# Optimization experiments

Measured on AMD Instinct MI355X. Metric: run time of the kernel, lower is better.

The kernel has to match this reference:

```python
import jax, jax.numpy as jnp
import numpy as np

EPS = jnp.finfo(jnp.float32).eps


def setup_inputs() -> dict:
    key = jax.random.key(0)
    k0, k1, k2 = jax.random.split(key, 3)
    B, N = 1, 4194304
    cloud_t0 = jax.random.normal(k0, (B, N, 3), dtype=jnp.float32)
    cloud_t1 = jax.random.normal(k1, (B, N, 3), dtype=jnp.float32)
    weights = jax.random.uniform(k2, (B, N), dtype=jnp.float32)
    return {"cloud_t0": cloud_t0, "cloud_t1": cloud_t1, "weights": weights}


def reference(cloud_t0, cloud_t1, weights):
    # use_epsilon_on_weights = False branch
    count_nonzero = jnp.sum(weights > 0.0, axis=-1)
    not_enough_points = count_nonzero < 3
    weights = weights + (not_enough_points.astype(weights.dtype) * EPS)[:, None]

    cum_wts = jnp.sum(weights, axis=-1)                      # (B,)
    w = weights[:, :, None]                                   # (B,N,1)
    mx = jnp.sum(cloud_t0 * w, axis=1) / cum_wts[:, None]     # (B,3) weighted centroid
    my = jnp.sum(cloud_t1 * w, axis=1) / cum_wts[:, None]
    Xc = cloud_t0 - mx[:, None, :]
    Yc = cloud_t1 - my[:, None, :]
    # weighted cross-covariance: (B,3,3)
    Sxy = jnp.einsum('bno,bni->boi', Yc * w, Xc) / cum_wts[:, None, None]

    U, D, Vh = jnp.linalg.svd(Sxy, full_matrices=False)       # torch.svd returns V = Vh^T
    V = jnp.swapaxes(Vh, -1, -2)

    # rank via torch.linalg.matrix_rank default tol: max_sv * max(m,n) * eps
    tol = D.max(axis=-1) * 3 * EPS
    rank = jnp.sum(D > tol[:, None], axis=-1)

    det_S = jnp.linalg.det(Sxy)
    det_mul = jnp.linalg.det(U) * jnp.linalg.det(V)
    sign_full = jnp.where(det_S < 0.0, -1.0, 1.0)             # rank == 3 case
    sign_def = jnp.where(jnp.isclose(det_mul, -1.0), -1.0, 1.0)  # rank == 2 case
    s = jnp.where(rank > 2, sign_full, sign_def)              # (B,)

    # R = U @ diag(1,1,s) @ V^T
    diag = jnp.stack([jnp.ones_like(s), jnp.ones_like(s), s], axis=-1)  # (B,3)
    R = jnp.einsum('boc,bc,bic->boi', U, diag, V)             # (B,3,3)
    t = my - jnp.einsum('boc,bc->bo', R, mx)                  # (B,3)

    B = R.shape[0]
    R4 = jnp.concatenate([R, jnp.zeros((B, 1, 3), R.dtype)], axis=1)    # (B,4,3)
    t4 = jnp.concatenate([t, jnp.ones((B, 1), t.dtype)], axis=-1)       # (B,4)
    T = jnp.concatenate([R4, t4[:, :, None]], axis=-1)        # (B,4,4)
    return T, not_enough_points
```

## Files before the change

### kernel.cpp

```cpp
#include <hip/hip_runtime.h>
#include <math.h>

#define NACC 32

typedef float f4 __attribute__((ext_vector_type(4)));


__device__ __forceinline__ void accum_point(float w, float x0, float x1, float x2,
                                            float y0, float y1, float y2, float* a) {
    a[0] += (w > 0.0f) ? 1.0f : 0.0f;
    a[1] += w;
    a[2] = fmaf(w, x0, a[2]); a[3] = fmaf(w, x1, a[3]); a[4] = fmaf(w, x2, a[4]);
    float wy0 = w * y0, wy1 = w * y1, wy2 = w * y2;
    a[5] += wy0; a[6] += wy1; a[7] += wy2;
    a[8]  = fmaf(wy0, x0, a[8]);  a[9]  = fmaf(wy0, x1, a[9]);  a[10] = fmaf(wy0, x2, a[10]);
    a[11] = fmaf(wy1, x0, a[11]); a[12] = fmaf(wy1, x1, a[12]); a[13] = fmaf(wy1, x2, a[13]);
    a[14] = fmaf(wy2, x0, a[14]); a[15] = fmaf(wy2, x1, a[15]); a[16] = fmaf(wy2, x2, a[16]);
    a[17] += x0; a[18] += x1; a[19] += x2;
    a[20] += y0; a[21] += y1; a[22] += y2;
    a[23] = fmaf(y0, x0, a[23]); a[24] = fmaf(y0, x1, a[24]); a[25] = fmaf(y0, x2, a[25]);
    a[26] = fmaf(y1, x0, a[26]); a[27] = fmaf(y1, x1, a[27]); a[28] = fmaf(y1, x2, a[28]);
    a[29] = fmaf(y2, x0, a[29]); a[30] = fmaf(y2, x1, a[30]); a[31] = fmaf(y2, x2, a[31]);
}

__device__ __forceinline__ double det3(const double m[3][3]) {
    return m[0][0] * (m[1][1] * m[2][2] - m[1][2] * m[2][1])
         - m[0][1] * (m[1][0] * m[2][2] - m[1][2] * m[2][0])
         + m[0][2] * (m[1][0] * m[2][1] - m[1][1] * m[2][0]);
}

__global__ __launch_bounds__(256) void kabsch_fused(
    const float* __restrict__ c0, const float* __restrict__ c1,
    const float* __restrict__ w, int N, float* __restrict__ acc32, int nblocks,
    unsigned* __restrict__ ticket, float* __restrict__ out) {
    __shared__ float wred[4][NACC];

    float a[NACC];
    #pragma unroll
    for (int i = 0; i < NACC; ++i) a[i] = 0.0f;

    const int t = threadIdx.x;
    const int lane = t & 63, wave = t >> 6;
    const f4* __restrict__ A4 = (const f4*)c0;
    const f4* __restrict__ B4 = (const f4*)c1;
    const f4* __restrict__ W4 = (const f4*)w;

    const int ngrp = N >> 2;
    const int stride = gridDim.x << 8;
    for (int g = (blockIdx.x << 8) + t; g < ngrp; g += stride) {
        int i3 = 3 * g;
        f4 a0 = A4[i3], a1 = A4[i3 + 1], a2 = A4[i3 + 2];
        f4 b0 = B4[i3], b1 = B4[i3 + 1], b2 = B4[i3 + 2];
        f4 vw = W4[g];
        accum_point(vw.x, a0.x, a0.y, a0.z, b0.x, b0.y, b0.z, a);
        accum_point(vw.y, a0.w, a1.x, a1.y, b0.w, b1.x, b1.y, a);
        accum_point(vw.z, a1.z, a1.w, a2.x, b1.z, b1.w, b2.x, a);
        accum_point(vw.w, a2.y, a2.z, a2.w, b2.y, b2.z, b2.w, a);
    }
    if (blockIdx.x == 0 && t == 0) {
        for (int i = (N >> 2) << 2; i < N; ++i)
            accum_point(w[i], c0[3*i], c0[3*i+1], c0[3*i+2],
                        c1[3*i], c1[3*i+1], c1[3*i+2], a);
    }

    {
        int hi;
        hi = lane & 1;
        #pragma unroll
        for (int i = 0; i < 16; ++i) {
            float send = hi ? a[i] : a[i + 16];
            float recv = __shfl_xor(send, 1, 64);
            a[i] = (hi ? a[i + 16] : a[i]) + recv;
        }
        hi = lane & 2;
        #pragma unroll
        for (int i = 0; i < 8; ++i) {
            float send = hi ? a[i] : a[i + 8];
            float recv = __shfl_xor(send, 2, 64);
            a[i] = (hi ? a[i + 8] : a[i]) + recv;
        }
        hi = lane & 4;
        #pragma unroll
        for (int i = 0; i < 4; ++i) {
            float send = hi ? a[i] : a[i + 4];
            float recv = __shfl_xor(send, 4, 64);
            a[i] = (hi ? a[i + 4] : a[i]) + recv;
        }
        hi = lane & 8;
        #pragma unroll
        for (int i = 0; i < 2; ++i) {
            float send = hi ? a[i] : a[i + 2];
            float recv = __shfl_xor(send, 8, 64);
            a[i] = (hi ? a[i + 2] : a[i]) + recv;
        }
        hi = lane & 16;
        {
            float send = hi ? a[0] : a[1];
            float recv = __shfl_xor(send, 16, 64);
            a[0] = (hi ? a[1] : a[0]) + recv;
        }
        a[0] += __shfl_xor(a[0], 32, 64);
    }
    if (lane < 32) {
        int acc = ((lane & 1) << 4) | ((lane & 2) << 2) | (lane & 4)
                | ((lane & 8) >> 2) | ((lane & 16) >> 4);
        wred[wave][acc] = a[0];
    }
    __syncthreads();

    if (t < NACC) {
        float val = wred[0][t] + wred[1][t] + wred[2][t] + wred[3][t];
        float* p = acc32 + t;
        asm volatile("global_atomic_add_f32 %0, %1, off"
                     :: "v"(p), "v"(val) : "memory");
    }
    asm volatile("s_waitcnt vmcnt(0)" ::: "memory");
    __syncthreads();
    __shared__ unsigned amlast;
    if (t == 0) amlast = atomicAdd(ticket, 1u);
    __syncthreads();
    if (amlast != (unsigned)(nblocks - 1)) return;

    __shared__ float tot[NACC];
    if (t < NACC) {
        float* p = acc32 + t;
        float zero = 0.0f, old;
        asm volatile("global_atomic_add_f32 %0, %1, %2, off sc0"
                     : "=&v"(old) : "v"(p), "v"(zero) : "memory");
        asm volatile("s_waitcnt vmcnt(0)" ::: "memory");
        tot[t] = old;
    }
    __syncthreads();
    if (t != 0) return;

    double d[NACC];
    #pragma unroll
    for (int i = 0; i < NACC; ++i) d[i] = (double)tot[i];

    const double EPSF = (double)1.1920929e-7f;
    double cnt = d[0];
    double W = d[1];
    double swx[3] = { d[2], d[3], d[4] };
    double swy[3] = { d[5], d[6], d[7] };
    double swyx[9];
    for (int i = 0; i < 9; ++i) swyx[i] = d[8 + i];
    bool nep = cnt < 3.0;
    if (nep) {
        W += EPSF * (double)N;
        for (int i = 0; i < 3; ++i) { swx[i] += EPSF * d[17 + i]; swy[i] += EPSF * d[20 + i]; }
        for (int i = 0; i < 9; ++i) swyx[i] += EPSF * d[23 + i];
    }

    double mx[3], my[3];
    for (int i = 0; i < 3; ++i) { mx[i] = swx[i] / W; my[i] = swy[i] / W; }
    double S[3][3];
    for (int o = 0; o < 3; ++o)
        for (int i = 0; i < 3; ++i)
            S[o][i] = swyx[o * 3 + i] / W - my[o] * mx[i];

    double Bm[3][3], V[3][3];
    for (int i = 0; i < 3; ++i)
        for (int j = 0; j < 3; ++j) {
            double acc = 0.0;
            for (int k = 0; k < 3; ++k) acc += S[k][i] * S[k][j];
            Bm[i][j] = acc;
            V[i][j] = (i == j) ? 1.0 : 0.0;
        }
    for (int sweep = 0; sweep < 30; ++sweep) {
        double off2 = Bm[0][1]*Bm[0][1] + Bm[0][2]*Bm[0][2] + Bm[1][2]*Bm[1][2];
        double diag2 = Bm[0][0]*Bm[0][0] + Bm[1][1]*Bm[1][1] + Bm[2][2]*Bm[2][2];
        if (off2 <= diag2 * 1e-32 + 1e-300) break;
        for (int pair = 0; pair < 3; ++pair) {
            int p = (pair == 2) ? 1 : 0;
            int q = (pair == 0) ? 1 : 2;
            double apq = Bm[p][q];
            if (fabs(apq) < 1e-300) continue;
            double theta = (Bm[q][q] - Bm[p][p]) / (2.0 * apq);
            double tt = ((theta >= 0.0) ? 1.0 : -1.0) / (fabs(theta) + sqrt(1.0 + theta * theta));
            double c = 1.0 / sqrt(1.0 + tt * tt);
            double sn = tt * c;
            for (int k = 0; k < 3; ++k) {
                double bkp = Bm[k][p], bkq = Bm[k][q];
                Bm[k][p] = c * bkp - sn * bkq;
                Bm[k][q] = sn * bkp + c * bkq;
            }
            for (int k = 0; k < 3; ++k) {
                double bpk = Bm[p][k], bqk = Bm[q][k];
                Bm[p][k] = c * bpk - sn * bqk;
                Bm[q][k] = sn * bpk + c * bqk;
            }
            for (int k = 0; k < 3; ++k) {
                double vkp = V[k][p], vkq = V[k][q];
                V[k][p] = c * vkp - sn * vkq;
                V[k][q] = sn * vkp + c * vkq;
            }
        }
    }
    double lam[3] = { Bm[0][0], Bm[1][1], Bm[2][2] };
    for (int i = 0; i < 2; ++i)
        for (int j = i + 1; j < 3; ++j)
            if (lam[j] > lam[i]) {
                double tl = lam[i]; lam[i] = lam[j]; lam[j] = tl;
                for (int k = 0; k < 3; ++k) { double tv = V[k][i]; V[k][i] = V[k][j]; V[k][j] = tv; }
            }
    double sig[3];
    for (int i = 0; i < 3; ++i) sig[i] = sqrt(fmax(lam[i], 0.0));

    double U[3][3];
    for (int i = 0; i < 3; ++i) {
        double u0 = S[0][0]*V[0][i] + S[0][1]*V[1][i] + S[0][2]*V[2][i];
        double u1 = S[1][0]*V[0][i] + S[1][1]*V[1][i] + S[1][2]*V[2][i];
        double u2 = S[2][0]*V[0][i] + S[2][1]*V[1][i] + S[2][2]*V[2][i];
        double nrm = sqrt(u0*u0 + u1*u1 + u2*u2);
        if (nrm > 1e-150) {
            U[0][i] = u0 / nrm; U[1][i] = u1 / nrm; U[2][i] = u2 / nrm;
        } else if (i == 0) {
            U[0][0] = 1.0; U[1][0] = 0.0; U[2][0] = 0.0;
        } else if (i == 1) {
            double e0 = (fabs(U[0][0]) < 0.9) ? 1.0 : 0.0;
            double e1 = 1.0 - e0;
            double dp = e0 * U[0][0] + e1 * U[1][0];
            double v0 = e0 - dp * U[0][0], v1 = e1 - dp * U[1][0], v2 = -dp * U[2][0];
            double n2 = sqrt(v0*v0 + v1*v1 + v2*v2);
            U[0][1] = v0 / n2; U[1][1] = v1 / n2; U[2][1] = v2 / n2;
        } else {
            U[0][2] = U[1][0]*U[2][1] - U[2][0]*U[1][1];
            U[1][2] = U[2][0]*U[0][1] - U[0][0]*U[2][1];
            U[2][2] = U[0][0]*U[1][1] - U[1][0]*U[0][1];
        }
    }

    double tol = sig[0] * 3.0 * EPSF;
    int rank = (sig[0] > tol) + (sig[1] > tol) + (sig[2] > tol);
    double detS = det3(S);
    double det_mul = det3(U) * det3(V);
    double sign_full = (detS < 0.0) ? -1.0 : 1.0;
    double sign_def = (fabs(det_mul + 1.0) <= 1.00001e-5) ? -1.0 : 1.0;
    double s = (rank > 2) ? sign_full : sign_def;

    double R[3][3];
    for (int o = 0; o < 3; ++o)
        for (int i = 0; i < 3; ++i)
            R[o][i] = U[o][0]*V[i][0] + U[o][1]*V[i][1] + s * U[o][2]*V[i][2];
    double tv[3];
    for (int o = 0; o < 3; ++o)
        tv[o] = my[o] - (R[o][0]*mx[0] + R[o][1]*mx[1] + R[o][2]*mx[2]);

    for (int o = 0; o < 3; ++o) {
        out[o * 4 + 0] = (float)R[o][0];
        out[o * 4 + 1] = (float)R[o][1];
        out[o * 4 + 2] = (float)R[o][2];
        out[o * 4 + 3] = (float)tv[o];
    }
    out[12] = 0.0f; out[13] = 0.0f; out[14] = 0.0f; out[15] = 1.0f;
    out[16] = nep ? 1.0f : 0.0f;
}

extern "C" void kernel_launch(void* const* d_in, const int* in_sizes, int n_in,
                              void* d_out, int out_size, void* d_ws, size_t ws_size,
                              hipStream_t stream) {
    const float* c0 = (const float*)d_in[0];
    const float* c1 = (const float*)d_in[1];
    const float* w  = (const float*)d_in[2];
    float* out = (float*)d_out;
    int N = in_sizes[2];

    int ngrp = N >> 2;
    int blocks = (ngrp + 255) >> 8;
    if (blocks > 1024) blocks = 1024;
    if (blocks < 1) blocks = 1;

    float* acc32 = (float*)d_ws;
    unsigned* ticket = (unsigned*)((char*)d_ws + NACC * sizeof(float));

    hipMemsetAsync(d_ws, 0, NACC * sizeof(float) + sizeof(unsigned), stream);
    kabsch_fused<<<blocks, 256, 0, stream>>>(c0, c1, w, N, acc32, blocks, ticket, out);
}
```

Baseline: 150.7 us.

## Software-prefetch next grid-stride tile and pad global atomic accumulators to separate lines

The grid-stride loop now loads the next iteration's coordinates and weights into registers before accumulating the current ones, so memory latency overlaps with the FMA work. Each of the 32 global accumulators gets its own 128-byte slot to avoid atomic contention on the same cache line, and launch bounds request one block per CU so the compiler may use more registers. This costs extra registers for the prefetch buffers, a larger memset, and may reduce occupancy.

```diff
diff --git a/kernel.cpp b/kernel.cpp
--- a/kernel.cpp
+++ b/kernel.cpp
@@ -2,6 +2,7 @@
 #include <math.h>
 
 #define NACC 32
+#define ACC_STRIDE 32
 
 typedef float f4 __attribute__((ext_vector_type(4)));
 
@@ -29,7 +30,7 @@
          + m[0][2] * (m[1][0] * m[2][1] - m[1][1] * m[2][0]);
 }
 
-__global__ __launch_bounds__(256) void kabsch_fused(
+__global__ __launch_bounds__(256, 1) void kabsch_fused(
     const float* __restrict__ c0, const float* __restrict__ c1,
     const float* __restrict__ w, int N, float* __restrict__ acc32, int nblocks,
     unsigned* __restrict__ ticket, float* __restrict__ out) {
@@ -47,15 +48,33 @@
 
     const int ngrp = N >> 2;
     const int stride = gridDim.x << 8;
-    for (int g = (blockIdx.x << 8) + t; g < ngrp; g += stride) {
-        int i3 = 3 * g;
-        f4 a0 = A4[i3], a1 = A4[i3 + 1], a2 = A4[i3 + 2];
-        f4 b0 = B4[i3], b1 = B4[i3 + 1], b2 = B4[i3 + 2];
-        f4 vw = W4[g];
-        accum_point(vw.x, a0.x, a0.y, a0.z, b0.x, b0.y, b0.z, a);
-        accum_point(vw.y, a0.w, a1.x, a1.y, b0.w, b1.x, b1.y, a);
-        accum_point(vw.z, a1.z, a1.w, a2.x, b1.z, b1.w, b2.x, a);
-        accum_point(vw.w, a2.y, a2.z, a2.w, b2.y, b2.z, b2.w, a);
+    {
+        int g = (blockIdx.x << 8) + t;
+        if (g < ngrp) {
+            const f4* pa = A4 + 3 * (size_t)g;
+            const f4* pb = B4 + 3 * (size_t)g;
+            f4 ca0 = pa[0], ca1 = pa[1], ca2 = pa[2];
+            f4 cb0 = pb[0], cb1 = pb[1], cb2 = pb[2];
+            f4 cw  = W4[g];
+            for (int gn = g + stride; ; gn += stride) {
+                const bool more = gn < ngrp;
+                f4 na0, na1, na2, nb0, nb1, nb2, nw;
+                if (more) {
+                    const f4* qa = A4 + 3 * (size_t)gn;
+                    const f4* qb = B4 + 3 * (size_t)gn;
+                    na0 = qa[0]; na1 = qa[1]; na2 = qa[2];
+                    nb0 = qb[0]; nb1 = qb[1]; nb2 = qb[2];
+                    nw  = W4[gn];
+                }
+                accum_point(cw.x, ca0.x, ca0.y, ca0.z, cb0.x, cb0.y, cb0.z, a);
+                accum_point(cw.y, ca0.w, ca1.x, ca1.y, cb0.w, cb1.x, cb1.y, a);
+                accum_point(cw.z, ca1.z, ca1.w, ca2.x, cb1.z, cb1.w, cb2.x, a);
+                accum_point(cw.w, ca2.y, ca2.z, ca2.w, cb2.y, cb2.z, cb2.w, a);
+                if (!more) break;
+                ca0 = na0; ca1 = na1; ca2 = na2;
+                cb0 = nb0; cb1 = nb1; cb2 = nb2; cw = nw;
+            }
+        }
     }
     if (blockIdx.x == 0 && t == 0) {
         for (int i = (N >> 2) << 2; i < N; ++i)
@@ -110,7 +129,7 @@
 
     if (t < NACC) {
         float val = wred[0][t] + wred[1][t] + wred[2][t] + wred[3][t];
-        float* p = acc32 + t;
+        float* p = acc32 + (t << 5);
         asm volatile("global_atomic_add_f32 %0, %1, off"
                      :: "v"(p), "v"(val) : "memory");
     }
@@ -123,7 +142,7 @@
 
     __shared__ float tot[NACC];
     if (t < NACC) {
-        float* p = acc32 + t;
+        float* p = acc32 + (t << 5);
         float zero = 0.0f, old;
         asm volatile("global_atomic_add_f32 %0, %1, %2, off sc0"
                      : "=&v"(old) : "v"(p), "v"(zero) : "memory");
@@ -271,8 +290,8 @@
     if (blocks < 1) blocks = 1;
 
     float* acc32 = (float*)d_ws;
-    unsigned* ticket = (unsigned*)((char*)d_ws + NACC * sizeof(float));
-
-    hipMemsetAsync(d_ws, 0, NACC * sizeof(float) + sizeof(unsigned), stream);
+    unsigned* ticket = (unsigned*)((char*)d_ws + NACC * ACC_STRIDE * sizeof(float));
+
+    hipMemsetAsync(d_ws, 0, NACC * ACC_STRIDE * sizeof(float) + sizeof(unsigned), stream);
     kabsch_fused<<<blocks, 256, 0, stream>>>(c0, c1, w, N, acc32, blocks, ticket, out);
 }
```

After: 146.6 us. 1.03x faster.

## Drop unweighted sums from hot loop, recompute only in rare fallback path

Applied to the files above, without the earlier changes.

The main streaming loop now accumulates only the 17 weighted sums and leaves out the 15 unweighted sums that only the rare not-enough-points case needs. When that case triggers, the last block rescans the clouds in double precision to get them. The loop also loads two groups per iteration to keep more loads in flight, each global atomic accumulator gets its own 128-byte slot, and the wave reduction becomes a plain butterfly per accumulator. This cuts per-point ALU work and register pressure, but the fallback rescan is serial over N within a single block.

```diff
diff --git a/kernel.cpp b/kernel.cpp
--- a/kernel.cpp
+++ b/kernel.cpp
@@ -1,7 +1,8 @@
 #include <hip/hip_runtime.h>
 #include <math.h>
 
-#define NACC 32
+#define NACC 17
+#define ACC_STRIDE 32
 
 typedef float f4 __attribute__((ext_vector_type(4)));
 
@@ -16,11 +17,6 @@
     a[8]  = fmaf(wy0, x0, a[8]);  a[9]  = fmaf(wy0, x1, a[9]);  a[10] = fmaf(wy0, x2, a[10]);
     a[11] = fmaf(wy1, x0, a[11]); a[12] = fmaf(wy1, x1, a[12]); a[13] = fmaf(wy1, x2, a[13]);
     a[14] = fmaf(wy2, x0, a[14]); a[15] = fmaf(wy2, x1, a[15]); a[16] = fmaf(wy2, x2, a[16]);
-    a[17] += x0; a[18] += x1; a[19] += x2;
-    a[20] += y0; a[21] += y1; a[22] += y2;
-    a[23] = fmaf(y0, x0, a[23]); a[24] = fmaf(y0, x1, a[24]); a[25] = fmaf(y0, x2, a[25]);
-    a[26] = fmaf(y1, x0, a[26]); a[27] = fmaf(y1, x1, a[27]); a[28] = fmaf(y1, x2, a[28]);
-    a[29] = fmaf(y2, x0, a[29]); a[30] = fmaf(y2, x1, a[30]); a[31] = fmaf(y2, x2, a[31]);
 }
 
 __device__ __forceinline__ double det3(const double m[3][3]) {
@@ -29,7 +25,7 @@
          + m[0][2] * (m[1][0] * m[2][1] - m[1][1] * m[2][0]);
 }
 
-__global__ __launch_bounds__(256) void kabsch_fused(
+__global__ __launch_bounds__(256, 1) void kabsch_fused(
     const float* __restrict__ c0, const float* __restrict__ c1,
     const float* __restrict__ w, int N, float* __restrict__ acc32, int nblocks,
     unsigned* __restrict__ ticket, float* __restrict__ out) {
@@ -46,16 +42,30 @@
     const f4* __restrict__ W4 = (const f4*)w;
 
     const int ngrp = N >> 2;
-    const int stride = gridDim.x << 8;
-    for (int g = (blockIdx.x << 8) + t; g < ngrp; g += stride) {
-        int i3 = 3 * g;
-        f4 a0 = A4[i3], a1 = A4[i3 + 1], a2 = A4[i3 + 2];
-        f4 b0 = B4[i3], b1 = B4[i3 + 1], b2 = B4[i3 + 2];
-        f4 vw = W4[g];
-        accum_point(vw.x, a0.x, a0.y, a0.z, b0.x, b0.y, b0.z, a);
-        accum_point(vw.y, a0.w, a1.x, a1.y, b0.w, b1.x, b1.y, a);
-        accum_point(vw.z, a1.z, a1.w, a2.x, b1.z, b1.w, b2.x, a);
-        accum_point(vw.w, a2.y, a2.z, a2.w, b2.y, b2.z, b2.w, a);
+    const int stride = gridDim.x << 9;
+    for (int g0 = (blockIdx.x << 9) + t; g0 < ngrp; g0 += stride) {
+        int g1 = g0 + 256;
+        bool h1 = g1 < ngrp;
+        int g1c = h1 ? g1 : g0;
+        const f4* pa0 = A4 + 3 * (size_t)g0;
+        const f4* pb0 = B4 + 3 * (size_t)g0;
+        const f4* pa1 = A4 + 3 * (size_t)g1c;
+        const f4* pb1 = B4 + 3 * (size_t)g1c;
+        f4 xa0 = pa0[0], xa1 = pa0[1], xa2 = pa0[2];
+        f4 xb0 = pb0[0], xb1 = pb0[1], xb2 = pb0[2];
+        f4 xw  = W4[g0];
+        f4 ya0 = pa1[0], ya1 = pa1[1], ya2 = pa1[2];
+        f4 yb0 = pb1[0], yb1 = pb1[1], yb2 = pb1[2];
+        f4 yw  = W4[g1c];
+        if (!h1) { yw.x = 0.0f; yw.y = 0.0f; yw.z = 0.0f; yw.w = 0.0f; }
+        accum_point(xw.x, xa0.x, xa0.y, xa0.z, xb0.x, xb0.y, xb0.z, a);
+        accum_point(xw.y, xa0.w, xa1.x, xa1.y, xb0.w, xb1.x, xb1.y, a);
+        accum_point(xw.z, xa1.z, xa1.w, xa2.x, xb1.z, xb1.w, xb2.x, a);
+        accum_point(xw.w, xa2.y, xa2.z, xa2.w, xb2.y, xb2.z, xb2.w, a);
+        accum_point(yw.x, ya0.x, ya0.y, ya0.z, yb0.x, yb0.y, yb0.z, a);
+        accum_point(yw.y, ya0.w, ya1.x, ya1.y, yb0.w, yb1.x, yb1.y, a);
+        accum_point(yw.z, ya1.z, ya1.w, ya2.x, yb1.z, yb1.w, yb2.x, a);
+        accum_point(yw.w, ya2.y, ya2.z, ya2.w, yb2.y, yb2.z, yb2.w, a);
     }
     if (blockIdx.x == 0 && t == 0) {
         for (int i = (N >> 2) << 2; i < N; ++i)
@@ -63,54 +73,26 @@
                         c1[3*i], c1[3*i+1], c1[3*i+2], a);
     }
 
-    {
-        int hi;
-        hi = lane & 1;
+    #pragma unroll
+    for (int i = 0; i < NACC; ++i) {
+        float v = a[i];
+        v += __shfl_xor(v, 1, 64);
+        v += __shfl_xor(v, 2, 64);
+        v += __shfl_xor(v, 4, 64);
+        v += __shfl_xor(v, 8, 64);
+        v += __shfl_xor(v, 16, 64);
+        v += __shfl_xor(v, 32, 64);
+        a[i] = v;
+    }
+    if (lane == 0) {
         #pragma unroll
-        for (int i = 0; i < 16; ++i) {
-            float send = hi ? a[i] : a[i + 16];
-            float recv = __shfl_xor(send, 1, 64);
-            a[i] = (hi ? a[i + 16] : a[i]) + recv;
-        }
-        hi = lane & 2;
-        #pragma unroll
-        for (int i = 0; i < 8; ++i) {
-            float send = hi ? a[i] : a[i + 8];
-            float recv = __shfl_xor(send, 2, 64);
-            a[i] = (hi ? a[i + 8] : a[i]) + recv;
-        }
-        hi = lane & 4;
-        #pragma unroll
-        for (int i = 0; i < 4; ++i) {
-            float send = hi ? a[i] : a[i + 4];
-            float recv = __shfl_xor(send, 4, 64);
-            a[i] = (hi ? a[i + 4] : a[i]) + recv;
-        }
-        hi = lane & 8;
-        #pragma unroll
-        for (int i = 0; i < 2; ++i) {
-            float send = hi ? a[i] : a[i + 2];
-            float recv = __shfl_xor(send, 8, 64);
-            a[i] = (hi ? a[i + 2] : a[i]) + recv;
-        }
-        hi = lane & 16;
-        {
-            float send = hi ? a[0] : a[1];
-            float recv = __shfl_xor(send, 16, 64);
-            a[0] = (hi ? a[1] : a[0]) + recv;
-        }
-        a[0] += __shfl_xor(a[0], 32, 64);
-    }
-    if (lane < 32) {
-        int acc = ((lane & 1) << 4) | ((lane & 2) << 2) | (lane & 4)
-                | ((lane & 8) >> 2) | ((lane & 16) >> 4);
-        wred[wave][acc] = a[0];
+        for (int i = 0; i < NACC; ++i) wred[wave][i] = a[i];
     }
     __syncthreads();
 
     if (t < NACC) {
         float val = wred[0][t] + wred[1][t] + wred[2][t] + wred[3][t];
-        float* p = acc32 + t;
+        float* p = acc32 + (t << 5);
         asm volatile("global_atomic_add_f32 %0, %1, off"
                      :: "v"(p), "v"(val) : "memory");
     }
@@ -123,7 +105,7 @@
 
     __shared__ float tot[NACC];
     if (t < NACC) {
-        float* p = acc32 + t;
+        float* p = acc32 + (t << 5);
         float zero = 0.0f, old;
         asm volatile("global_atomic_add_f32 %0, %1, %2, off sc0"
                      : "=&v"(old) : "v"(p), "v"(zero) : "memory");
@@ -131,6 +113,33 @@
         tot[t] = old;
     }
     __syncthreads();
+
+    bool nep = (tot[0] < 3.0f);
+    __shared__ double csm[4][15];
+    if (nep) {
+        double cs[15];
+        #pragma unroll
+        for (int k = 0; k < 15; ++k) cs[k] = 0.0;
+        for (int i = t; i < N; i += 256) {
+            double x0 = c0[3*i], x1 = c0[3*i+1], x2 = c0[3*i+2];
+            double y0 = c1[3*i], y1 = c1[3*i+1], y2 = c1[3*i+2];
+            cs[0] += x0; cs[1] += x1; cs[2] += x2;
+            cs[3] += y0; cs[4] += y1; cs[5] += y2;
+            cs[6]  += y0*x0; cs[7]  += y0*x1; cs[8]  += y0*x2;
+            cs[9]  += y1*x0; cs[10] += y1*x1; cs[11] += y1*x2;
+            cs[12] += y2*x0; cs[13] += y2*x1; cs[14] += y2*x2;
+        }
+        #pragma unroll
+        for (int off = 32; off > 0; off >>= 1) {
+            #pragma unroll
+            for (int k = 0; k < 15; ++k) cs[k] += __shfl_down(cs[k], off, 64);
+        }
+        if (lane == 0) {
+            #pragma unroll
+            for (int k = 0; k < 15; ++k) csm[wave][k] = cs[k];
+        }
+        __syncthreads();
+    }
     if (t != 0) return;
 
     double d[NACC];
@@ -138,17 +147,18 @@
     for (int i = 0; i < NACC; ++i) d[i] = (double)tot[i];
 
     const double EPSF = (double)1.1920929e-7f;
-    double cnt = d[0];
     double W = d[1];
     double swx[3] = { d[2], d[3], d[4] };
     double swy[3] = { d[5], d[6], d[7] };
     double swyx[9];
     for (int i = 0; i < 9; ++i) swyx[i] = d[8 + i];
-    bool nep = cnt < 3.0;
     if (nep) {
+        double corr[15];
+        for (int k = 0; k < 15; ++k)
+            corr[k] = csm[0][k] + csm[1][k] + csm[2][k] + csm[3][k];
         W += EPSF * (double)N;
-        for (int i = 0; i < 3; ++i) { swx[i] += EPSF * d[17 + i]; swy[i] += EPSF * d[20 + i]; }
-        for (int i = 0; i < 9; ++i) swyx[i] += EPSF * d[23 + i];
+        for (int i = 0; i < 3; ++i) { swx[i] += EPSF * corr[i]; swy[i] += EPSF * corr[3 + i]; }
+        for (int i = 0; i < 9; ++i) swyx[i] += EPSF * corr[6 + i];
     }
 
     double mx[3], my[3];
@@ -266,13 +276,13 @@
     int N = in_sizes[2];
 
     int ngrp = N >> 2;
-    int blocks = (ngrp + 255) >> 8;
+    int blocks = (ngrp + 511) >> 9;
     if (blocks > 1024) blocks = 1024;
     if (blocks < 1) blocks = 1;
 
     float* acc32 = (float*)d_ws;
-    unsigned* ticket = (unsigned*)((char*)d_ws + NACC * sizeof(float));
-
-    hipMemsetAsync(d_ws, 0, NACC * sizeof(float) + sizeof(unsigned), stream);
+    unsigned* ticket = (unsigned*)((char*)d_ws + NACC * ACC_STRIDE * sizeof(float));
+
+    hipMemsetAsync(d_ws, 0, NACC * ACC_STRIDE * sizeof(float) + sizeof(unsigned), stream);
     kabsch_fused<<<blocks, 256, 0, stream>>>(c0, c1, w, N, acc32, blocks, ticket, out);
 }
```

New measurement: 154.9 us. 1.03x slower.
